# Performance work log

Hardware: AMD Instinct MI355X
Metric: run time of the kernel (lower is better)

The kernel has to match this reference:

```python
import math
import jax, jax.numpy as jnp
import numpy as np

B, SX, SY, D, H = 2, 1024, 1024, 1024, 16
FULL = 1536   # padded (full_q == full_k) frame length for the two-source attention
N_CTX = 2048  # causal bias buffer size
HD = D // H
LENS_X = np.array([1024, 700])
LENS_Y = np.array([1024, 850])


def _heads(t):
    b, s, d = t.shape
    return t.reshape(b, s, H, HD).transpose(0, 2, 1, 3)  # [B,H,S,HD]


def _merge(t):
    b, h, s, hd = t.shape
    return t.transpose(0, 2, 1, 3).reshape(b, s, h * hd)


def setup_inputs() -> dict:
    key = jax.random.key(0)
    ks = jax.random.split(key, 8)
    s = 0.02
    # ragged pack/unpack index lists: take = positions in the FULL frame, fill = positions in the shrunk frame
    x_take_b = np.concatenate([np.full(l, b, np.int32) for b, l in enumerate(LENS_X)])
    x_take_p = np.concatenate([(FULL - l + np.arange(l)).astype(np.int32) for l in LENS_X])  # right-aligned
    x_fill_b = x_take_b.copy()
    x_fill_p = np.concatenate([np.arange(l, dtype=np.int32) for l in LENS_X])
    y_take_b = np.concatenate([np.full(l, b, np.int32) for b, l in enumerate(LENS_Y)])
    y_take_p = np.concatenate([np.arange(l, dtype=np.int32) for l in LENS_Y])  # left-aligned
    y_fill_b = y_take_b.copy()
    y_fill_p = y_take_p.copy()
    # additive padding mask for the self-attention over shrunk x
    mask = np.full((B, 1, 1, SX), -10000.0, np.float32)
    for b, l in enumerate(LENS_X):
        mask[b, :, :, :l] = 0.0
    return {
        "x": jax.random.normal(ks[0], (B, SX, D), jnp.float32),
        "y": jax.random.normal(ks[1], (B, SY, D), jnp.float32),
        "attention_mask_x": jnp.asarray(mask),
        "W_attn": jax.random.normal(ks[2], (D, 3 * D), jnp.float32) * s,
        "b_attn": jnp.zeros((3 * D,), jnp.float32),
        "W_2a": jax.random.normal(ks[3], (D, D), jnp.float32) * s,
        "b_2a": jnp.zeros((D,), jnp.float32),
        "W_2b": jax.random.normal(ks[4], (D, 2 * D), jnp.float32) * s,
        "b_2b": jnp.zeros((2 * D,), jnp.float32),
        "W_proj": jax.random.normal(ks[5], (2 * D, D), jnp.float32) * s,
        "b_proj": jnp.zeros((D,), jnp.float32),
        "x_take_b": jnp.asarray(x_take_b), "x_take_p": jnp.asarray(x_take_p),
        "x_fill_b": jnp.asarray(x_fill_b), "x_fill_p": jnp.asarray(x_fill_p),
        "y_take_b": jnp.asarray(y_take_b), "y_take_p": jnp.asarray(y_take_p),
        "y_fill_b": jnp.asarray(y_fill_b), "y_fill_p": jnp.asarray(y_fill_p),
    }


def reference(x, y, attention_mask_x, W_attn, b_attn, W_2a, b_2a, W_2b, b_2b,
              W_proj, b_proj, x_take_b, x_take_p, x_fill_b, x_fill_p,
              y_take_b, y_take_p, y_fill_b, y_fill_p):
    causal = jnp.tril(jnp.ones((N_CTX, N_CTX), jnp.float32))
    inv_sqrt = 1.0 / math.sqrt(HD)

    # --- branch 1: causal self-attention on shrunk x ---
    qkv = x @ W_attn + b_attn
    q, k, v = jnp.split(qkv, 3, axis=2)
    q, k, v = _heads(q), _heads(k), _heads(v)
    w = jnp.einsum('bhqd,bhkd->bhqk', q, k) * inv_sqrt  # [B,H,SX,SX]
    b1 = causal[:SX, :SX]
    w = w * b1 - 10000.0 * (1.0 - b1) + attention_mask_x
    a = jnp.einsum('bhqk,bhkd->bhqd', jax.nn.softmax(w, axis=-1), v)
    a = _merge(a)  # [B,SX,D]

    # --- branch 2: two-source attention with ragged expand/shrink ---
    q2 = _heads(x @ W_2a + b_2a)                      # [B,H,SX,HD]
    k2, v2 = jnp.split(y @ W_2b + b_2b, 2, axis=2)
    k2, v2 = _heads(k2), _heads(v2)                   # [B,H,SY,HD]
    w2 = jnp.einsum('bhqd,bhkd->bhqk', q2, k2)        # [B,H,SX,SY] (unscaled yet)
    # expand key dim: shrunk SY -> FULL
    temp = jnp.zeros((B, H, SX, FULL), w2.dtype)
    temp = temp.at[y_take_b, :, :, y_take_p].set(w2[y_fill_b, :, :, y_fill_p])
    # expand query dim: shrunk SX -> FULL
    new_w = jnp.zeros((B, H, FULL, FULL), w2.dtype)
    new_w = new_w.at[x_take_b, :, x_take_p, :].set(temp[x_fill_b, :, x_fill_p, :])
    new_v = jnp.zeros((B, H, FULL, HD), v2.dtype)
    new_v = new_v.at[y_take_b, :, y_take_p, :].set(v2[y_fill_b, :, y_fill_p, :])
    kmask = jnp.full((B, 1, 1, FULL), -10000.0, w2.dtype)
    kmask = kmask.at[y_take_b, :, :, y_take_p].set(0.0)
    new_w = new_w * inv_sqrt
    b2 = causal[:FULL, :FULL]  # ns-nd == 0 since full_q == full_k
    new_w = new_w * b2 - 10000.0 * (1.0 - b2) + kmask
    a2 = jnp.einsum('bhqk,bhkd->bhqd', jax.nn.softmax(new_w, axis=-1), new_v)  # [B,H,FULL,HD]
    # shrink query dim back: FULL -> SX
    a2s = jnp.zeros((B, H, SX, HD), a2.dtype)
    a2s = a2s.at[x_fill_b, :, x_fill_p, :].set(a2[x_take_b, :, x_take_p, :])
    a2m = _merge(a2s)  # [B,SX,D]

    out = jnp.concatenate([a, a2m], axis=2) @ W_proj + b_proj  # [B,SX,D]
    return out
```

## Files before the change

### kernel.cpp

```cpp
#include <hip/hip_runtime.h>
#include <hip/hip_bf16.h>

typedef __bf16 bf16;
typedef __attribute__((ext_vector_type(4))) __bf16 bf16x4;
typedef __attribute__((ext_vector_type(8))) __bf16 bf16x8;
typedef __attribute__((ext_vector_type(4))) float floatx4;

__device__ __forceinline__ void gl_lds16(const bf16* g, bf16* l) {
  __builtin_amdgcn_global_load_lds(
      (const __attribute__((address_space(1))) void*)g,
      (__attribute__((address_space(3))) void*)l, 16, 0, 0);
}

__global__ __launch_bounds__(256) void sentinel_kernel(float* out, int n, float code) {
  int i = blockIdx.x * 256 + threadIdx.x;
  if (i < n) out[i] = code;
}

struct TP { const float* W; bf16* WT; int K; int N; int bxn; int bid0; };

__global__ __launch_bounds__(256) void prep_kernel(TP t0, TP t1, TP t2, TP t3,
                                                   const float* __restrict__ x,
                                                   const float* __restrict__ y,
                                                   bf16* __restrict__ xb,
                                                   bf16* __restrict__ yb) {
  __shared__ bf16 tile[32][33];
  int bid = blockIdx.x;
  if (bid < 8192) {
    TP t = t0;
    if (bid >= t3.bid0) t = t3;
    else if (bid >= t2.bid0) t = t2;
    else if (bid >= t1.bid0) t = t1;
    int rb = bid - t.bid0;
    int bx = rb % t.bxn, by = rb / t.bxn;
    int n0 = bx * 32, k0 = by * 32;
    int tx = threadIdx.x & 31, ty = threadIdx.x >> 5;
#pragma unroll
    for (int i = 0; i < 32; i += 8)
      tile[ty + i][tx] = (bf16)t.W[(size_t)(k0 + ty + i) * t.N + n0 + tx];
    __syncthreads();
#pragma unroll
    for (int i = 0; i < 32; i += 8)
      t.WT[(size_t)(n0 + ty + i) * t.K + k0 + tx] = tile[tx][ty + i];
  } else {
    long base = (long)(bid - 8192) * 4096 + (long)threadIdx.x * 16;
    const float* src = x; bf16* dst = xb; long idx = base;
    if (base >= 2097152) { src = y; dst = yb; idx = base - 2097152; }
    floatx4 v0 = *(const floatx4*)(src + idx);
    floatx4 v1 = *(const floatx4*)(src + idx + 4);
    floatx4 v2 = *(const floatx4*)(src + idx + 8);
    floatx4 v3 = *(const floatx4*)(src + idx + 12);
    bf16x8 o0, o1;
#pragma unroll
    for (int i = 0; i < 4; ++i) {
      o0[i] = (bf16)v0[i]; o0[4 + i] = (bf16)v1[i];
      o1[i] = (bf16)v2[i]; o1[4 + i] = (bf16)v3[i];
    }
    *(bf16x8*)(dst + idx) = o0;
    *(bf16x8*)(dst + idx + 8) = o1;
  }
}

struct GP { const bf16* A; const bf16* WT; const float* bias; bf16* C; bf16* VT;
            int N; int ldc; int vcol0; int bxn; int bid0; };

__global__ __launch_bounds__(256) void proj3_kernel(GP g0, GP g1, GP g2) {
  __shared__ __attribute__((aligned(16))) bf16 As[128 * 32];
  __shared__ __attribute__((aligned(16))) bf16 Bs[128 * 32];
  int bid = blockIdx.x;
  GP g = g0;
  if (bid >= g2.bid0) g = g2;
  else if (bid >= g1.bid0) g = g1;
  int rb = bid - g.bid0;
  int row0 = (rb / g.bxn) * 128, col0 = (rb % g.bxn) * 128;
  const int K = 1024;
  int tid = threadIdx.x;
  int lane = tid & 63, wave = tid >> 6;
  int quad = lane >> 4, l16 = lane & 15;
  int wm = wave >> 1, wn = wave & 1;
  floatx4 acc[4][4] = {};
  for (int k0 = 0; k0 < K; k0 += 32) {
#pragma unroll
    for (int s = 0; s < 2; ++s) {
      int chunk = s * 256 + tid;
      int r = chunk >> 2, c = (chunk & 3) * 8;
      gl_lds16(g.WT + (size_t)(col0 + r) * K + k0 + c, Bs + (size_t)chunk * 8);
      gl_lds16(g.A + (size_t)(row0 + r) * K + k0 + c, As + (size_t)chunk * 8);
    }
    __syncthreads();
    bf16x8 afr[4], bfr[4];
#pragma unroll
    for (int r = 0; r < 4; ++r)
      afr[r] = *(const bf16x8*)(As + (wm * 64 + r * 16 + l16) * 32 + quad * 8);
#pragma unroll
    for (int c = 0; c < 4; ++c)
      bfr[c] = *(const bf16x8*)(Bs + (wn * 64 + c * 16 + l16) * 32 + quad * 8);
#pragma unroll
    for (int r = 0; r < 4; ++r)
#pragma unroll
      for (int c = 0; c < 4; ++c)
        acc[r][c] = __builtin_amdgcn_mfma_f32_16x16x32_bf16(afr[r], bfr[c], acc[r][c], 0, 0, 0);
    __syncthreads();
  }
  int inV = (col0 >= g.vcol0);
#pragma unroll
  for (int c = 0; c < 4; ++c) {
    int gcol = col0 + wn * 64 + c * 16 + l16;
    float bv = g.bias[gcol];
    if (inV) {
      int vcol = gcol - g.vcol0;
      int hh = vcol >> 6, dd = vcol & 63;
#pragma unroll
      for (int r = 0; r < 4; ++r) {
        int row = row0 + wm * 64 + r * 16 + quad * 4;
        int bb = row >> 10, key = row & 1023;
        bf16x4 pk;
#pragma unroll
        for (int e = 0; e < 4; ++e) pk[e] = (bf16)(acc[r][c][e] + bv);
        *(bf16x4*)(g.VT + ((size_t)((bb << 4) + hh)) * 65536 + (size_t)dd * 1024 + key) = pk;
      }
    } else {
#pragma unroll
      for (int r = 0; r < 4; ++r) {
        int grow = row0 + wm * 64 + r * 16 + quad * 4;
#pragma unroll
        for (int e = 0; e < 4; ++e)
          g.C[(size_t)(grow + e) * g.ldc + gcol] = (bf16)(acc[r][c][e] + bv);
      }
    }
  }
}

__global__ __launch_bounds__(256) void gemm_out_kernel(const bf16* __restrict__ A,
                                                       const bf16* __restrict__ WT,
                                                       const float* __restrict__ bias,
                                                       float* __restrict__ C,
                                                       int N, int K) {
  __shared__ __attribute__((aligned(16))) bf16 As[64 * 32];
  __shared__ __attribute__((aligned(16))) bf16 Bs[64 * 32];
  int tid = threadIdx.x;
  int lane = tid & 63, wave = tid >> 6;
  int quad = lane >> 4, l16 = lane & 15;
  int row0 = blockIdx.y * 64, col0 = blockIdx.x * 64;
  floatx4 acc[4] = {};
  for (int k0 = 0; k0 < K; k0 += 32) {
    int r = tid >> 2, c = (tid & 3) * 8;
    gl_lds16(A + (size_t)(row0 + r) * K + k0 + c, As + (size_t)tid * 8);
    gl_lds16(WT + (size_t)(col0 + r) * K + k0 + c, Bs + (size_t)tid * 8);
    __syncthreads();
    bf16x8 af = *(const bf16x8*)(As + (wave * 16 + l16) * 32 + quad * 8);
#pragma unroll
    for (int nt = 0; nt < 4; ++nt) {
      bf16x8 bf = *(const bf16x8*)(Bs + (nt * 16 + l16) * 32 + quad * 8);
      acc[nt] = __builtin_amdgcn_mfma_f32_16x16x32_bf16(af, bf, acc[nt], 0, 0, 0);
    }
    __syncthreads();
  }
#pragma unroll
  for (int nt = 0; nt < 4; ++nt) {
    int gcol = col0 + nt * 16 + l16;
    float bv = bias[gcol];
#pragma unroll
    for (int e = 0; e < 4; ++e) {
      int grow = row0 + wave * 16 + quad * 4 + e;
      C[(size_t)grow * N + gcol] = acc[nt][e] + bv;
    }
  }
}

struct AP {
  const bf16* Q; const bf16* K; const bf16* VT; bf16* O;
  int qstride, kstride, ostride;
  long qbatch, kbatch, obatch;
  int coff0, coff1, klen0, klen1, qv0, qv1;
};

__global__ __launch_bounds__(256) void attn2x_kernel(AP a0, AP a1, float scale) {
  __shared__ __attribute__((aligned(16))) bf16 Ks[2][64 * 64];
  __shared__ __attribute__((aligned(16))) bf16 Vs[2][64 * 64];
  __shared__ __attribute__((aligned(16))) bf16 Ps[4][32 * 68];
  AP a = (blockIdx.x >> 8) ? a1 : a0;
  int tid = threadIdx.x;
  int lane = tid & 63, w = tid >> 6;
  int quad = lane >> 4, l16 = lane & 15;
  int r = blockIdx.x & 255;
  int b = r >> 7, h = (r >> 3) & 15, qh = (r >> 1) & 3, rnd = r & 1;
  int qt = rnd ? (7 - qh) : qh;
  int coff = b ? a.coff1 : a.coff0;
  int klen = b ? a.klen1 : a.klen0;
  int qv = b ? a.qv1 : a.qv0;
  int qbase = qt * 128;
  const bf16* Q   = a.Q + (size_t)b * a.qbatch + h * 64;
  const bf16* Kp  = a.K + (size_t)b * a.kbatch + h * 64;
  const bf16* VTp = a.VT + (size_t)(b * 16 + h) * 65536;
  bf16* O = a.O + (size_t)b * a.obatch + h * 64;

  bf16x8 aq[2][2];
#pragma unroll
  for (int mt = 0; mt < 2; ++mt) {
    int qrow = qbase + w * 32 + mt * 16 + l16;
    aq[mt][0] = *(const bf16x8*)(Q + (size_t)qrow * a.qstride + quad * 8);
    aq[mt][1] = *(const bf16x8*)(Q + (size_t)qrow * a.qstride + 32 + quad * 8);
  }

  floatx4 o[2][4] = {};
  float part[2][4] = {};

  int kend = klen < qbase + 128 + coff ? klen : qbase + 128 + coff;
  int nblk = (kend + 63) >> 6;
  int wqmin = qbase + w * 32;
  int wkend0 = wqmin + 32 + coff;
  int wkend = klen < wkend0 ? klen : wkend0;

  const float KSC = scale * 1.44269504f;
  const float KOFF = -5.77078016f;

  auto stage = [&](int buf, int j0) {
#pragma unroll
    for (int half = 0; half < 2; ++half) {
      int sl = half * 256 + tid;
      int row = sl >> 3, ch = sl & 7;
      gl_lds16(Kp + (size_t)(j0 + row) * a.kstride + ((ch ^ (row & 7)) * 8),
               Ks[buf] + (size_t)sl * 8);
      gl_lds16(VTp + (size_t)row * 1024 + j0 + ((ch ^ (row & 7)) * 8),
               Vs[buf] + (size_t)sl * 8);
    }
  };

  stage(0, 0);
  for (int t = 0; t < nblk; ++t) {
    int j0 = t * 64;
    __syncthreads();
    if (t + 1 < nblk) stage((t + 1) & 1, j0 + 64);
    if (j0 >= wkend) continue;
    const bf16* Kt = Ks[t & 1];
    const bf16* Vt = Vs[t & 1];

    floatx4 sv[2][4];
#pragma unroll
    for (int mt = 0; mt < 2; ++mt)
#pragma unroll
      for (int nt = 0; nt < 4; ++nt) {
        int key = nt * 16 + l16;
        int sl0 = key * 8 + (quad ^ (key & 7));
        int sl1 = key * 8 + ((quad + 4) ^ (key & 7));
        bf16x8 bk0 = *(const bf16x8*)(Kt + (size_t)sl0 * 8);
        bf16x8 bk1 = *(const bf16x8*)(Kt + (size_t)sl1 * 8);
        floatx4 z = {};
        z = __builtin_amdgcn_mfma_f32_16x16x32_bf16(aq[mt][0], bk0, z, 0, 0, 0);
        z = __builtin_amdgcn_mfma_f32_16x16x32_bf16(aq[mt][1], bk1, z, 0, 0, 0);
        sv[mt][nt] = z;
      }
    bool fullv = (j0 + 63 <= wqmin + coff) && (j0 + 63 < klen);
#pragma unroll
    for (int mt = 0; mt < 2; ++mt)
#pragma unroll
      for (int nt = 0; nt < 4; ++nt)
#pragma unroll
        for (int e = 0; e < 4; ++e) {
          float arg = fmaf(sv[mt][nt][e], KSC, KOFF);
          if (!fullv) {
            int j = j0 + nt * 16 + l16;
            int qi = wqmin + mt * 16 + quad * 4 + e;
            arg = (j <= qi + coff && j < klen) ? arg : -60.0f;
          }
          float p = exp2f(arg);
          Ps[w][(mt * 16 + quad * 4 + e) * 68 + nt * 16 + l16] = (bf16)p;
          part[mt][e] += p;
        }
#pragma unroll
    for (int mt = 0; mt < 2; ++mt) {
      bf16x8 pa0 = *(const bf16x8*)(Ps[w] + (mt * 16 + l16) * 68 + quad * 8);
      bf16x8 pa1 = *(const bf16x8*)(Ps[w] + (mt * 16 + l16) * 68 + 32 + quad * 8);
#pragma unroll
      for (int ct = 0; ct < 4; ++ct) {
        int dd = ct * 16 + l16;
        int sl0 = dd * 8 + (quad ^ (dd & 7));
        int sl1 = dd * 8 + ((quad + 4) ^ (dd & 7));
        bf16x8 bv0 = *(const bf16x8*)(Vt + (size_t)sl0 * 8);
        bf16x8 bv1 = *(const bf16x8*)(Vt + (size_t)sl1 * 8);
        o[mt][ct] = __builtin_amdgcn_mfma_f32_16x16x32_bf16(pa0, bv0, o[mt][ct], 0, 0, 0);
        o[mt][ct] = __builtin_amdgcn_mfma_f32_16x16x32_bf16(pa1, bv1, o[mt][ct], 0, 0, 0);
      }
    }
  }
#pragma unroll
  for (int off = 1; off < 16; off <<= 1)
#pragma unroll
    for (int mt = 0; mt < 2; ++mt)
#pragma unroll
      for (int e = 0; e < 4; ++e)
        part[mt][e] += __shfl_xor(part[mt][e], off);
#pragma unroll
  for (int mt = 0; mt < 2; ++mt)
#pragma unroll
    for (int ct = 0; ct < 4; ++ct)
#pragma unroll
      for (int e = 0; e < 4; ++e) {
        int qi = wqmin + mt * 16 + quad * 4 + e;
        float val = o[mt][ct][e] / part[mt][e];
        if (qi >= qv) val = 0.f;
        O[(size_t)qi * a.ostride + ct * 16 + l16] = (bf16)val;
      }
}

extern "C" void kernel_launch(void* const* d_in, const int* in_sizes, int n_in,
                              void* d_out, int out_size, void* d_ws, size_t ws_size,
                              hipStream_t stream) {
  const float* x      = (const float*)d_in[0];
  const float* y      = (const float*)d_in[1];
  const float* W_attn = (const float*)d_in[3];
  const float* b_attn = (const float*)d_in[4];
  const float* W_2a   = (const float*)d_in[5];
  const float* b_2a   = (const float*)d_in[6];
  const float* W_2b   = (const float*)d_in[7];
  const float* b_2b   = (const float*)d_in[8];
  const float* W_proj = (const float*)d_in[9];
  const float* b_proj = (const float*)d_in[10];
  bf16* ws = (bf16*)d_ws;
  float* out = (float*)d_out;

  const int LX0 = 1024, LX1 = 700, LY0 = 1024, LY1 = 850;
  const float scale = 0.125f;
  const size_t WS_FAST = (size_t)25165824 * 2;

  if (ws_size < WS_FAST) {
    sentinel_kernel<<<(out_size + 255) / 256, 256, 0, stream>>>(
        out, out_size, (float)(ws_size >> 20) + 10.0f);
    return;
  }

  bf16* qk1  = ws;
  bf16* q2   = ws + (size_t) 4194304;
  bf16* k2   = ws + (size_t) 6291456;
  bf16* VT1  = ws + (size_t) 8388608;
  bf16* VT2  = ws + (size_t)10485760;
  bf16* xb   = ws + (size_t)12582912;
  bf16* yb   = ws + (size_t)14680064;
  bf16* cat  = ws + (size_t)12582912;
  bf16* WaT  = ws + (size_t)16777216;
  bf16* W2aT = ws + (size_t)19922944;
  bf16* W2bT = ws + (size_t)20971520;
  bf16* WpT  = ws + (size_t)23068672;

  TP t0 = {W_attn, WaT, 1024, 3072, 96, 0};
  TP t1 = {W_2a, W2aT, 1024, 1024, 32, 3072};
  TP t2 = {W_2b, W2bT, 1024, 2048, 64, 4096};
  TP t3 = {W_proj, WpT, 2048, 1024, 32, 6144};
  prep_kernel<<<9216, 256, 0, stream>>>(t0, t1, t2, t3, x, y, xb, yb);

  GP g0 = {xb, WaT, b_attn, qk1, VT1, 3072, 2048, 2048, 24, 0};
  GP g1 = {xb, W2aT, b_2a, q2, nullptr, 1024, 1024, 1 << 30, 8, 384};
  GP g2 = {yb, W2bT, b_2b, k2, VT2, 2048, 1024, 1024, 16, 512};
  proj3_kernel<<<768, 256, 0, stream>>>(g0, g1, g2);

  AP a0 = {qk1, qk1 + 1024, VT1, cat, 2048, 2048, 2048,
           (long)1024 * 2048, (long)1024 * 2048, (long)1024 * 2048,
           0, 0, LX0, LX1, 1024, 1024};
  AP a1 = {q2, k2, VT2, cat + 1024, 1024, 1024, 2048,
           (long)1024 * 1024, (long)1024 * 1024, (long)1024 * 2048,
           1536 - LX0, 1536 - LX1, LY0, LY1, LX0, LX1};
  attn2x_kernel<<<512, 256, 0, stream>>>(a0, a1, scale);

  gemm_out_kernel<<<dim3(16, 32), 256, 0, stream>>>(cat, WpT, b_proj, out, 1024, 2048);
}
```

Before: 247.6 us.

## Use eight 16-row waves per attention block with transposed MFMA scores

The attention kernel now runs 512 threads per block, so each of eight waves handles 16 query rows instead of four waves handling 32. The score MFMA operands are swapped so each lane owns one query row's scores. This lets the softmax row sum reduce with two shuffles and lets P be written to LDS as packed 4-element vectors, with vectorized output stores. The load-balancing permutation of query tiles is dropped, and the change trades fewer registers per wave and more waves in flight for more waves competing for the same K/V tiles.

```diff
diff --git a/kernel.cpp b/kernel.cpp
--- a/kernel.cpp
+++ b/kernel.cpp
@@ -175,56 +175,47 @@
   int coff0, coff1, klen0, klen1, qv0, qv1;
 };
 
-__global__ __launch_bounds__(256) void attn2x_kernel(AP a0, AP a1, float scale) {
+__global__ __launch_bounds__(512) void attn2x_kernel(AP a0, AP a1, float scale) {
   __shared__ __attribute__((aligned(16))) bf16 Ks[2][64 * 64];
   __shared__ __attribute__((aligned(16))) bf16 Vs[2][64 * 64];
-  __shared__ __attribute__((aligned(16))) bf16 Ps[4][32 * 68];
+  __shared__ __attribute__((aligned(16))) bf16 Ps[8][16 * 72];
   AP a = (blockIdx.x >> 8) ? a1 : a0;
   int tid = threadIdx.x;
   int lane = tid & 63, w = tid >> 6;
   int quad = lane >> 4, l16 = lane & 15;
   int r = blockIdx.x & 255;
-  int b = r >> 7, h = (r >> 3) & 15, qh = (r >> 1) & 3, rnd = r & 1;
-  int qt = rnd ? (7 - qh) : qh;
+  int b = r >> 7, h = (r >> 3) & 15, qt = r & 7;
   int coff = b ? a.coff1 : a.coff0;
   int klen = b ? a.klen1 : a.klen0;
   int qv = b ? a.qv1 : a.qv0;
   int qbase = qt * 128;
+  int wq0 = qbase + w * 16;
+  int qi = wq0 + l16;
   const bf16* Q   = a.Q + (size_t)b * a.qbatch + h * 64;
   const bf16* Kp  = a.K + (size_t)b * a.kbatch + h * 64;
   const bf16* VTp = a.VT + (size_t)(b * 16 + h) * 65536;
   bf16* O = a.O + (size_t)b * a.obatch + h * 64;
 
-  bf16x8 aq[2][2];
-#pragma unroll
-  for (int mt = 0; mt < 2; ++mt) {
-    int qrow = qbase + w * 32 + mt * 16 + l16;
-    aq[mt][0] = *(const bf16x8*)(Q + (size_t)qrow * a.qstride + quad * 8);
-    aq[mt][1] = *(const bf16x8*)(Q + (size_t)qrow * a.qstride + 32 + quad * 8);
-  }
-
-  floatx4 o[2][4] = {};
-  float part[2][4] = {};
+  bf16x8 aq0 = *(const bf16x8*)(Q + (size_t)qi * a.qstride + quad * 8);
+  bf16x8 aq1 = *(const bf16x8*)(Q + (size_t)qi * a.qstride + 32 + quad * 8);
+
+  floatx4 o[4] = {};
+  float part = 0.f;
 
   int kend = klen < qbase + 128 + coff ? klen : qbase + 128 + coff;
   int nblk = (kend + 63) >> 6;
-  int wqmin = qbase + w * 32;
-  int wkend0 = wqmin + 32 + coff;
+  int wkend0 = wq0 + 16 + coff;
   int wkend = klen < wkend0 ? klen : wkend0;
 
   const float KSC = scale * 1.44269504f;
   const float KOFF = -5.77078016f;
 
   auto stage = [&](int buf, int j0) {
-#pragma unroll
-    for (int half = 0; half < 2; ++half) {
-      int sl = half * 256 + tid;
-      int row = sl >> 3, ch = sl & 7;
-      gl_lds16(Kp + (size_t)(j0 + row) * a.kstride + ((ch ^ (row & 7)) * 8),
-               Ks[buf] + (size_t)sl * 8);
-      gl_lds16(VTp + (size_t)row * 1024 + j0 + ((ch ^ (row & 7)) * 8),
-               Vs[buf] + (size_t)sl * 8);
-    }
+    int row = tid >> 3, ch = tid & 7;
+    gl_lds16(Kp + (size_t)(j0 + row) * a.kstride + ((ch ^ (row & 7)) * 8),
+             Ks[buf] + (size_t)tid * 8);
+    gl_lds16(VTp + (size_t)row * 1024 + j0 + ((ch ^ (row & 7)) * 8),
+             Vs[buf] + (size_t)tid * 8);
   };
 
   stage(0, 0);
@@ -236,72 +227,63 @@
     const bf16* Kt = Ks[t & 1];
     const bf16* Vt = Vs[t & 1];
 
-    floatx4 sv[2][4];
-#pragma unroll
-    for (int mt = 0; mt < 2; ++mt)
-#pragma unroll
-      for (int nt = 0; nt < 4; ++nt) {
-        int key = nt * 16 + l16;
-        int sl0 = key * 8 + (quad ^ (key & 7));
-        int sl1 = key * 8 + ((quad + 4) ^ (key & 7));
-        bf16x8 bk0 = *(const bf16x8*)(Kt + (size_t)sl0 * 8);
-        bf16x8 bk1 = *(const bf16x8*)(Kt + (size_t)sl1 * 8);
-        floatx4 z = {};
-        z = __builtin_amdgcn_mfma_f32_16x16x32_bf16(aq[mt][0], bk0, z, 0, 0, 0);
-        z = __builtin_amdgcn_mfma_f32_16x16x32_bf16(aq[mt][1], bk1, z, 0, 0, 0);
-        sv[mt][nt] = z;
+    floatx4 sv[4];
+#pragma unroll
+    for (int nt = 0; nt < 4; ++nt) {
+      int key = nt * 16 + l16;
+      int sl0 = key * 8 + (quad ^ (key & 7));
+      int sl1 = key * 8 + ((quad + 4) ^ (key & 7));
+      bf16x8 bk0 = *(const bf16x8*)(Kt + (size_t)sl0 * 8);
+      bf16x8 bk1 = *(const bf16x8*)(Kt + (size_t)sl1 * 8);
+      floatx4 z = {};
+      z = __builtin_amdgcn_mfma_f32_16x16x32_bf16(bk0, aq0, z, 0, 0, 0);
+      z = __builtin_amdgcn_mfma_f32_16x16x32_bf16(bk1, aq1, z, 0, 0, 0);
+      sv[nt] = z;
+    }
+    bool fullv = (j0 + 63 <= wq0 + coff) && (j0 + 63 < klen);
+#pragma unroll
+    for (int nt = 0; nt < 4; ++nt) {
+      bf16x4 pk;
+#pragma unroll
+      for (int e = 0; e < 4; ++e) {
+        float arg = fmaf(sv[nt][e], KSC, KOFF);
+        if (!fullv) {
+          int j = j0 + nt * 16 + quad * 4 + e;
+          arg = (j <= qi + coff && j < klen) ? arg : -60.0f;
+        }
+        float p = exp2f(arg);
+        part += p;
+        pk[e] = (bf16)p;
       }
-    bool fullv = (j0 + 63 <= wqmin + coff) && (j0 + 63 < klen);
-#pragma unroll
-    for (int mt = 0; mt < 2; ++mt)
-#pragma unroll
-      for (int nt = 0; nt < 4; ++nt)
-#pragma unroll
-        for (int e = 0; e < 4; ++e) {
-          float arg = fmaf(sv[mt][nt][e], KSC, KOFF);
-          if (!fullv) {
-            int j = j0 + nt * 16 + l16;
-            int qi = wqmin + mt * 16 + quad * 4 + e;
-            arg = (j <= qi + coff && j < klen) ? arg : -60.0f;
-          }
-          float p = exp2f(arg);
-          Ps[w][(mt * 16 + quad * 4 + e) * 68 + nt * 16 + l16] = (bf16)p;
-          part[mt][e] += p;
-        }
-#pragma unroll
-    for (int mt = 0; mt < 2; ++mt) {
-      bf16x8 pa0 = *(const bf16x8*)(Ps[w] + (mt * 16 + l16) * 68 + quad * 8);
-      bf16x8 pa1 = *(const bf16x8*)(Ps[w] + (mt * 16 + l16) * 68 + 32 + quad * 8);
-#pragma unroll
-      for (int ct = 0; ct < 4; ++ct) {
-        int dd = ct * 16 + l16;
-        int sl0 = dd * 8 + (quad ^ (dd & 7));
-        int sl1 = dd * 8 + ((quad + 4) ^ (dd & 7));
-        bf16x8 bv0 = *(const bf16x8*)(Vt + (size_t)sl0 * 8);
-        bf16x8 bv1 = *(const bf16x8*)(Vt + (size_t)sl1 * 8);
-        o[mt][ct] = __builtin_amdgcn_mfma_f32_16x16x32_bf16(pa0, bv0, o[mt][ct], 0, 0, 0);
-        o[mt][ct] = __builtin_amdgcn_mfma_f32_16x16x32_bf16(pa1, bv1, o[mt][ct], 0, 0, 0);
-      }
-    }
-  }
-#pragma unroll
-  for (int off = 1; off < 16; off <<= 1)
-#pragma unroll
-    for (int mt = 0; mt < 2; ++mt)
-#pragma unroll
-      for (int e = 0; e < 4; ++e)
-        part[mt][e] += __shfl_xor(part[mt][e], off);
-#pragma unroll
-  for (int mt = 0; mt < 2; ++mt)
-#pragma unroll
-    for (int ct = 0; ct < 4; ++ct)
-#pragma unroll
-      for (int e = 0; e < 4; ++e) {
-        int qi = wqmin + mt * 16 + quad * 4 + e;
-        float val = o[mt][ct][e] / part[mt][e];
-        if (qi >= qv) val = 0.f;
-        O[(size_t)qi * a.ostride + ct * 16 + l16] = (bf16)val;
-      }
+      *(bf16x4*)(Ps[w] + l16 * 72 + nt * 16 + quad * 4) = pk;
+    }
+    bf16x8 pb0 = *(const bf16x8*)(Ps[w] + l16 * 72 + quad * 8);
+    bf16x8 pb1 = *(const bf16x8*)(Ps[w] + l16 * 72 + 32 + quad * 8);
+#pragma unroll
+    for (int ct = 0; ct < 4; ++ct) {
+      int dd = ct * 16 + l16;
+      int sl0 = dd * 8 + (quad ^ (dd & 7));
+      int sl1 = dd * 8 + ((quad + 4) ^ (dd & 7));
+      bf16x8 va0 = *(const bf16x8*)(Vt + (size_t)sl0 * 8);
+      bf16x8 va1 = *(const bf16x8*)(Vt + (size_t)sl1 * 8);
+      o[ct] = __builtin_amdgcn_mfma_f32_16x16x32_bf16(va0, pb0, o[ct], 0, 0, 0);
+      o[ct] = __builtin_amdgcn_mfma_f32_16x16x32_bf16(va1, pb1, o[ct], 0, 0, 0);
+    }
+  }
+  part += __shfl_xor(part, 16);
+  part += __shfl_xor(part, 32);
+  float rinv = 1.0f / part;
+#pragma unroll
+  for (int ct = 0; ct < 4; ++ct) {
+    bf16x4 pk;
+#pragma unroll
+    for (int e = 0; e < 4; ++e) {
+      float val = o[ct][e] * rinv;
+      if (qi >= qv) val = 0.f;
+      pk[e] = (bf16)val;
+    }
+    *(bf16x4*)(O + (size_t)qi * a.ostride + ct * 16 + quad * 4) = pk;
+  }
 }
 
 extern "C" void kernel_launch(void* const* d_in, const int* in_sizes, int n_in,
@@ -360,7 +342,7 @@
   AP a1 = {q2, k2, VT2, cat + 1024, 1024, 1024, 2048,
            (long)1024 * 1024, (long)1024 * 1024, (long)1024 * 2048,
            1536 - LX0, 1536 - LX1, LY0, LY1, LX0, LX1};
-  attn2x_kernel<<<512, 256, 0, stream>>>(a0, a1, scale);
+  attn2x_kernel<<<512, 512, 0, stream>>>(a0, a1, scale);
 
   gemm_out_kernel<<<dim3(16, 32), 256, 0, stream>>>(cat, WpT, b_proj, out, 1024, 2048);
 }
```

Measured after the change: 236.5 us. 4.5% less time.
